# Kernel optimization log

Measured on AMD Instinct MI355X. Metric: run time of the kernel, lower is better.

Reference implementation:

```python
import jax, jax.numpy as jnp
import numpy as np

B, D, C = 8192, 2048, 1000
NUM_IDS = 256
MSEL_W, ORTH_W, CONS_W = 0.5, 0.1, 0.1


def setup_inputs() -> dict:
    key = jax.random.key(0)
    ks = jax.random.split(key, 7)
    return {
        "feat_shared": jax.random.normal(ks[0], (B, D), dtype=jnp.float32),
        "dee1": jax.random.normal(ks[1], (B, D), dtype=jnp.float32),
        "dee2": jax.random.normal(ks[2], (B, D), dtype=jnp.float32),
        "dee3": jax.random.normal(ks[3], (B, D), dtype=jnp.float32),
        "logits": jax.random.normal(ks[4], (B, C), dtype=jnp.float32),
        "labels": jax.random.randint(ks[5], (B,), 0, NUM_IDS, dtype=jnp.int32),
        "modal_ids": jax.random.randint(ks[6], (B,), 0, 2, dtype=jnp.int32),
    }


def _l2norm(x):
    return x / jnp.sqrt(jnp.sum(x * x, axis=1, keepdims=True)).clip(1e-12)


def _msel(features, labels, modal_ids):
    f = _l2norm(features)
    m_rgb = (modal_ids == 0).astype(f.dtype)  # [B]
    m_sar = (modal_ids == 1).astype(f.dtype)
    # per-label per-modal sums and counts via segment_sum (fixed NUM_IDS segments)
    sum_rgb = jax.ops.segment_sum(f * m_rgb[:, None], labels, num_segments=NUM_IDS)  # [L,D]
    sum_sar = jax.ops.segment_sum(f * m_sar[:, None], labels, num_segments=NUM_IDS)
    n_rgb = jax.ops.segment_sum(m_rgb, labels, num_segments=NUM_IDS)  # [L]
    n_sar = jax.ops.segment_sum(m_sar, labels, num_segments=NUM_IDS)
    c_rgb = sum_rgb / jnp.maximum(n_rgb, 1.0)[:, None]
    c_sar = sum_sar / jnp.maximum(n_sar, 1.0)[:, None]
    dist_cross = 1.0 - jnp.sum(c_rgb * c_sar, axis=1)
    # mean of Gram(f_rgb, f_rgb) == center_rgb . center_rgb (includes diagonal), same math
    dist_intra = 1.0 - jnp.sum(c_rgb * c_rgb, axis=1)
    valid = (n_rgb >= 2.0) & (n_sar >= 1.0)
    per_label = jnp.where(valid, (dist_cross - dist_intra) ** 2, 0.0)
    count = jnp.sum(valid.astype(f.dtype))
    return jnp.where(count > 0, jnp.sum(per_label) / jnp.maximum(count, 1.0), 0.0)


def _orth(f1, f2, f3):
    n1, n2, n3 = _l2norm(f1), _l2norm(f2), _l2norm(f3)
    s12 = jnp.mean(jnp.abs(jnp.sum(n1 * n2, axis=1)))
    s13 = jnp.mean(jnp.abs(jnp.sum(n1 * n3, axis=1)))
    s23 = jnp.mean(jnp.abs(jnp.sum(n2 * n3, axis=1)))
    return s12 + s13 + s23


def _consistency(logits, modal_ids):
    probs = jax.nn.softmax(logits, axis=1)  # [B,C]
    m_rgb = (modal_ids == 0).astype(probs.dtype)
    m_sar = (modal_ids == 1).astype(probs.dtype)
    n_rgb = jnp.sum(m_rgb)
    n_sar = jnp.sum(m_sar)
    p_rgb = jnp.sum(probs * m_rgb[:, None], axis=0) / jnp.maximum(n_rgb, 1.0)
    p_sar = jnp.sum(probs * m_sar[:, None], axis=0) / jnp.maximum(n_sar, 1.0)
    lr, ls = jnp.log(p_rgb), jnp.log(p_sar)
    # F.kl_div(log p, q, 'sum') = sum q*(log q - log p)
    kl = 0.5 * (jnp.sum(p_sar * (ls - lr)) + jnp.sum(p_rgb * (lr - ls)))
    return jnp.where((n_rgb > 0) & (n_sar > 0), kl, 0.0)


def reference(feat_shared, dee1, dee2, dee3, logits, labels, modal_ids):
    loss = MSEL_W * _msel(feat_shared, labels, modal_ids)
    loss = loss + ORTH_W * _orth(dee1, dee2, dee3)
    loss = loss + CONS_W * _consistency(logits, modal_ids)
    return loss
```

## Files before the change

kernel.cpp:

```cpp
#include <hip/hip_runtime.h>
#include <math.h>

#define B_   8192
#define D_   2048
#define C_   1000
#define L_   256
#define BIN_CAP 64

#define BIN_BLK  32
#define ORTH_BLK 512
#define NORM_BLK 128
#define CONS_BLK 128
#define GRID_ (BIN_BLK + ORTH_BLK + NORM_BLK + CONS_BLK)
#define ORTH_WAVES (ORTH_BLK * 4)

typedef unsigned short bf16raw;

__device__ __forceinline__ float bflo(unsigned int u) { return __uint_as_float(u << 16); }
__device__ __forceinline__ float bfhi(unsigned int u) { return __uint_as_float(u & 0xffff0000u); }

__device__ __forceinline__ bf16raw f2b(float f) {
  unsigned int x = __float_as_uint(f);
  unsigned int r = (x + 0x7fffu + ((x >> 16) & 1u)) >> 16;
  return (bf16raw)r;
}

__device__ __forceinline__ void dec8(uint4 u, float* x) {
  x[0] = bflo(u.x); x[1] = bfhi(u.x);
  x[2] = bflo(u.y); x[3] = bfhi(u.y);
  x[4] = bflo(u.z); x[5] = bfhi(u.z);
  x[6] = bflo(u.w); x[7] = bfhi(u.w);
}

__device__ __forceinline__ float waveSum(float v) {
#pragma unroll
  for (int off = 32; off > 0; off >>= 1) v += __shfl_xor(v, off, 64);
  return v;
}

__device__ __forceinline__ float blockSum(float v, float* lds4) {
  v = waveSum(v);
  const int wave = threadIdx.x >> 6;
  if ((threadIdx.x & 63) == 0) lds4[wave] = v;
  __syncthreads();
  v = lds4[0] + lds4[1] + lds4[2] + lds4[3];
  __syncthreads();
  return v;
}

__device__ __forceinline__ int detect_isb(const unsigned int* feat_words, float* lds4) {
  const unsigned int w = feat_words[threadIdx.x];
  const float a = fabsf(bflo(w));
  float hit = (a > 1e-3f && a < 10.f) ? 1.f : 0.f;
  hit = blockSum(hit, lds4);
  return hit > 128.f ? 1 : 0;
}

__global__ __launch_bounds__(256) void init_kernel(int* counts, float* accs,
                                                   float* p_final) {
  const int t = blockIdx.x * 256 + threadIdx.x;
  if (t < 2 * L_) counts[t] = 0;
  if (t < 16) accs[t] = 0.f;
  if (t < 2 * C_) p_final[t] = 0.f;
}

__device__ __forceinline__ void ldrow3(const bf16raw* pa, const bf16raw* pb,
                                       const bf16raw* pc, size_t base, int lane,
                                       uint4 (&A)[4], uint4 (&Bv)[4], uint4 (&Cv)[4]) {
  const uint4* qa = (const uint4*)(pa + base);
  const uint4* qb = (const uint4*)(pb + base);
  const uint4* qc = (const uint4*)(pc + base);
#pragma unroll
  for (int j = 0; j < 4; ++j) A[j] = qa[j * 64 + lane];
#pragma unroll
  for (int j = 0; j < 4; ++j) Bv[j] = qb[j * 64 + lane];
#pragma unroll
  for (int j = 0; j < 4; ++j) Cv[j] = qc[j * 64 + lane];
}

__device__ __forceinline__ void orth_rowacc(const uint4 (&A)[4], const uint4 (&Bv)[4],
                                            const uint4 (&Cv)[4], float (&v)[6]) {
#pragma unroll
  for (int j = 0; j < 4; ++j) {
    float a[8], b[8], c[8];
    dec8(A[j], a); dec8(Bv[j], b); dec8(Cv[j], c);
#pragma unroll
    for (int k = 0; k < 8; ++k) {
      v[0] += a[k] * a[k]; v[1] += b[k] * b[k]; v[2] += c[k] * c[k];
      v[3] += a[k] * b[k]; v[4] += a[k] * c[k]; v[5] += b[k] * c[k];
    }
  }
}

__device__ __forceinline__ float ssq4(const uint4 (&X)[4]) {
  float ss = 0.f;
#pragma unroll
  for (int j = 0; j < 4; ++j) {
    float x[8]; dec8(X[j], x);
#pragma unroll
    for (int k = 0; k < 8; ++k) ss += x[k] * x[k];
  }
  return ss;
}

__device__ __forceinline__ void loadlogits_f32(const void* logits, int r, int lane,
                                               float (&x)[16]) {
#pragma unroll
  for (int kk = 0; kk < 4; ++kk) {
    const int idx = lane + (kk << 6);
    if (idx < (C_ / 4)) {
      const float4 w = ((const float4*)((const float*)logits + (size_t)r * C_))[idx];
      x[4 * kk + 0] = w.x; x[4 * kk + 1] = w.y;
      x[4 * kk + 2] = w.z; x[4 * kk + 3] = w.w;
    } else {
      x[4 * kk + 0] = -INFINITY; x[4 * kk + 1] = -INFINITY;
      x[4 * kk + 2] = -INFINITY; x[4 * kk + 3] = -INFINITY;
    }
  }
}

__device__ __forceinline__ void softmax_acc(float (&x)[16], int m, float (&accA)[16],
                                            float (&accB)[16]) {
  float mx = -INFINITY;
#pragma unroll
  for (int k = 0; k < 16; ++k) mx = fmaxf(mx, x[k]);
#pragma unroll
  for (int off = 32; off > 0; off >>= 1) mx = fmaxf(mx, __shfl_xor(mx, off, 64));
  float s = 0.f;
#pragma unroll
  for (int k = 0; k < 16; ++k) { x[k] = expf(x[k] - mx); s += x[k]; }
#pragma unroll
  for (int off = 32; off > 0; off >>= 1) s += __shfl_xor(s, off, 64);
  const float inv = 1.f / s;
  if (m == 0) {
#pragma unroll
    for (int k = 0; k < 16; ++k) accA[k] += x[k] * inv;
  } else {
#pragma unroll
    for (int k = 0; k < 16; ++k) accB[k] += x[k] * inv;
  }
}

__global__ __launch_bounds__(256) void fused_main_kernel(
    const void* feat, const void* f1, const void* f2, const void* f3,
    const void* logits, const int* labels, const int* modal,
    int* counts, int* rowlist, float* orth_part, float* norms, float* p_final) {
  __shared__ float wacc[4][2][1024];
  __shared__ float lds4[4];
  const int t = threadIdx.x;
  const int wave = t >> 6, lane = t & 63;
  const int isb = detect_isb((const unsigned int*)feat, lds4);
  const int bx = blockIdx.x;

  if (bx < BIN_BLK) {
    const int r = bx * 256 + t;
    const int m = modal[r] ? 1 : 0;
    int lb = labels[r]; lb = lb < 0 ? 0 : (lb >= L_ ? L_ - 1 : lb);
    const int key = m * L_ + lb;
    const int idx = atomicAdd(&counts[key], 1);
    if (idx < BIN_CAP) rowlist[key * BIN_CAP + idx] = r;
  } else if (bx < BIN_BLK + ORTH_BLK) {
    const int gw = (bx - BIN_BLK) * 4 + wave;
    float s12 = 0.f, s13 = 0.f, s23 = 0.f;
    if (isb) {
      const bf16raw* pa = (const bf16raw*)f1;
      const bf16raw* pb = (const bf16raw*)f2;
      const bf16raw* pc = (const bf16raw*)f3;
      for (int r = 0; r < 4; ++r) {
        const size_t base = ((size_t)gw * 4 + r) * D_;
        uint4 A[4], Bv[4], Cv[4];
        ldrow3(pa, pb, pc, base, lane, A, Bv, Cv);
        float v[6] = {0.f, 0.f, 0.f, 0.f, 0.f, 0.f};
        orth_rowacc(A, Bv, Cv, v);
#pragma unroll
        for (int off = 32; off > 0; off >>= 1) {
#pragma unroll
          for (int j = 0; j < 6; ++j) v[j] += __shfl_xor(v[j], off, 64);
        }
        const float q1 = fmaxf(sqrtf(v[0]), 1e-12f);
        const float q2 = fmaxf(sqrtf(v[1]), 1e-12f);
        const float q3 = fmaxf(sqrtf(v[2]), 1e-12f);
        s12 += fabsf(v[3]) / (q1 * q2);
        s13 += fabsf(v[4]) / (q1 * q3);
        s23 += fabsf(v[5]) / (q2 * q3);
      }
    } else {
      for (int r = 0; r < 4; ++r) {
        const size_t base = ((size_t)gw * 4 + r) * D_;
        const float4* qa = (const float4*)((const float*)f1 + base);
        const float4* qb = (const float4*)((const float*)f2 + base);
        const float4* qc = (const float4*)((const float*)f3 + base);
        float v[6] = {0.f, 0.f, 0.f, 0.f, 0.f, 0.f};
#pragma unroll
        for (int h = 0; h < 8; ++h) {
          const float4 a4 = qa[h * 64 + lane];
          const float4 b4 = qb[h * 64 + lane];
          const float4 c4 = qc[h * 64 + lane];
          const float a[4] = {a4.x, a4.y, a4.z, a4.w};
          const float b[4] = {b4.x, b4.y, b4.z, b4.w};
          const float c[4] = {c4.x, c4.y, c4.z, c4.w};
#pragma unroll
          for (int k = 0; k < 4; ++k) {
            v[0] += a[k] * a[k]; v[1] += b[k] * b[k]; v[2] += c[k] * c[k];
            v[3] += a[k] * b[k]; v[4] += a[k] * c[k]; v[5] += b[k] * c[k];
          }
        }
#pragma unroll
        for (int off = 32; off > 0; off >>= 1) {
#pragma unroll
          for (int j = 0; j < 6; ++j) v[j] += __shfl_xor(v[j], off, 64);
        }
        const float q1 = fmaxf(sqrtf(v[0]), 1e-12f);
        const float q2 = fmaxf(sqrtf(v[1]), 1e-12f);
        const float q3 = fmaxf(sqrtf(v[2]), 1e-12f);
        s12 += fabsf(v[3]) / (q1 * q2);
        s13 += fabsf(v[4]) / (q1 * q3);
        s23 += fabsf(v[5]) / (q2 * q3);
      }
    }
    if (lane == 0) {
      orth_part[gw] = s12;
      orth_part[ORTH_WAVES + gw] = s13;
      orth_part[2 * ORTH_WAVES + gw] = s23;
    }
  } else if (bx < BIN_BLK + ORTH_BLK + NORM_BLK) {
    const int gw = (bx - BIN_BLK - ORTH_BLK) * 4 + wave;
    const size_t base0 = (size_t)gw * (16 * D_);
    if (isb) {
      const bf16raw* pf = (const bf16raw*)feat;
      for (int r = 0; r < 16; ++r) {
        const uint4* q = (const uint4*)(pf + base0 + (size_t)r * D_);
        uint4 X[4];
#pragma unroll
        for (int j = 0; j < 4; ++j) X[j] = q[j * 64 + lane];
        float ss = ssq4(X);
        ss = waveSum(ss);
        if (lane == 0) norms[gw * 16 + r] = 1.f / fmaxf(sqrtf(ss), 1e-12f);
      }
    } else {
      for (int r = 0; r < 16; ++r) {
        const float4* q = (const float4*)((const float*)feat + base0 + (size_t)r * D_);
        float ss = 0.f;
#pragma unroll
        for (int j = 0; j < 8; ++j) {
          const float4 w = q[j * 64 + lane];
          ss += w.x * w.x + w.y * w.y + w.z * w.z + w.w * w.w;
        }
        ss = waveSum(ss);
        if (lane == 0) norms[gw * 16 + r] = 1.f / fmaxf(sqrtf(ss), 1e-12f);
      }
    }
  } else {
    const int cb = bx - BIN_BLK - ORTH_BLK - NORM_BLK;
    const int rbase = cb * 64 + wave * 16;
    float accA[16], accB[16];
#pragma unroll
    for (int k = 0; k < 16; ++k) { accA[k] = 0.f; accB[k] = 0.f; }
    if (isb) {
      const bf16raw* pl = (const bf16raw*)logits;
      uint4 W0a, W1a;
      uint4 W0b = make_uint4(0u, 0u, 0u, 0u), W1b = make_uint4(0u, 0u, 0u, 0u);
      int ma, mb = 0;
      {
        const uint4* q = (const uint4*)(pl + (size_t)rbase * C_);
        W0a = q[lane];
        W1a = (lane < 61) ? q[64 + lane] : make_uint4(0u, 0u, 0u, 0u);
        ma = modal[rbase];
      }
      for (int i = 0; i < 16; ++i) {
        if (i < 15) {
          const int rn = rbase + i + 1;
          const uint4* q = (const uint4*)(pl + (size_t)rn * C_);
          W0b = q[lane];
          W1b = (lane < 61) ? q[64 + lane] : make_uint4(0u, 0u, 0u, 0u);
          mb = modal[rn];
        }
        float x[16];
        dec8(W0a, x);
        if (lane < 61) {
          float xx[8]; dec8(W1a, xx);
#pragma unroll
          for (int k = 0; k < 8; ++k) x[8 + k] = xx[k];
        } else {
#pragma unroll
          for (int k = 0; k < 8; ++k) x[8 + k] = -INFINITY;
        }
        softmax_acc(x, ma, accA, accB);
        W0a = W0b; W1a = W1b; ma = mb;
      }
#pragma unroll
      for (int k = 0; k < 16; ++k) {
        const int c = (k < 8) ? (8 * lane + k) : (512 + 8 * lane + (k - 8));
        wacc[wave][0][c] = accA[k];
        wacc[wave][1][c] = accB[k];
      }
    } else {
      float xa[16], xb[16];
      int ma, mb = 0;
      loadlogits_f32(logits, rbase, lane, xa);
      ma = modal[rbase];
      for (int i = 0; i < 16; ++i) {
        if (i < 15) {
          loadlogits_f32(logits, rbase + i + 1, lane, xb);
          mb = modal[rbase + i + 1];
        }
        softmax_acc(xa, ma, accA, accB);
#pragma unroll
        for (int k = 0; k < 16; ++k) xa[k] = xb[k];
        ma = mb;
      }
#pragma unroll
      for (int k = 0; k < 16; ++k) {
        const int c = 4 * (lane + ((k >> 2) << 6)) + (k & 3);
        wacc[wave][0][c] = accA[k];
        wacc[wave][1][c] = accB[k];
      }
    }
    __syncthreads();
    for (int e = t; e < 2 * C_; e += 256) {
      const int m = (e < C_) ? 0 : 1;
      const int c = e - m * C_;
      atomicAdd(&p_final[e],
                wacc[0][m][c] + wacc[1][m][c] + wacc[2][m][c] + wacc[3][m][c]);
    }
  }
}

__global__ __launch_bounds__(256) void label_kernel(const void* feat, const int* counts,
                                                    const int* rowlist, const float* norms,
                                                    float* accs) {
  __shared__ float lds4[4];
  const int l = blockIdx.x;
  const int t = threadIdx.x;
  const int isb = detect_isb((const unsigned int*)feat, lds4);
  const int nr_true = counts[l];
  const int ns_true = counts[L_ + l];
  const int nr = nr_true < BIN_CAP ? nr_true : BIN_CAP;
  const int ns = ns_true < BIN_CAP ? ns_true : BIN_CAP;
  const int tot = nr + ns;
  float accR[8], accS[8];
#pragma unroll
  for (int j = 0; j < 8; ++j) { accR[j] = 0.f; accS[j] = 0.f; }

  if (tot > 0) {
    auto rowAt = [&](int i) -> int {
      const int key = (i < nr) ? l : (L_ + l);
      const int idx = (i < nr) ? i : (i - nr);
      return rowlist[key * BIN_CAP + idx];
    };
    if (isb) {
      const bf16raw* pf = (const bf16raw*)feat;
      const int r0 = rowAt(0);
      uint4 qa = ((const uint4*)(pf + (size_t)r0 * D_))[t];
      float na = norms[r0];
      uint4 qb = make_uint4(0u, 0u, 0u, 0u);
      float nb2 = 0.f;
      if (tot > 1) {
        const int r1 = rowAt(1);
        qb = ((const uint4*)(pf + (size_t)r1 * D_))[t];
        nb2 = norms[r1];
      }
      for (int i = 0; i < tot; i += 2) {
        uint4 qc = make_uint4(0u, 0u, 0u, 0u), qd = make_uint4(0u, 0u, 0u, 0u);
        float nc = 0.f, nd = 0.f;
        if (i + 2 < tot) {
          const int rc = rowAt(i + 2);
          qc = ((const uint4*)(pf + (size_t)rc * D_))[t];
          nc = norms[rc];
        }
        if (i + 3 < tot) {
          const int rd = rowAt(i + 3);
          qd = ((const uint4*)(pf + (size_t)rd * D_))[t];
          nd = norms[rd];
        }
        {
          float x[8]; dec8(qa, x);
          if (i < nr) {
#pragma unroll
            for (int j = 0; j < 8; ++j) accR[j] += x[j] * na;
          } else {
#pragma unroll
            for (int j = 0; j < 8; ++j) accS[j] += x[j] * na;
          }
        }
        if (i + 1 < tot) {
          float x[8]; dec8(qb, x);
          if (i + 1 < nr) {
#pragma unroll
            for (int j = 0; j < 8; ++j) accR[j] += x[j] * nb2;
          } else {
#pragma unroll
            for (int j = 0; j < 8; ++j) accS[j] += x[j] * nb2;
          }
        }
        qa = qc; qb = qd; na = nc; nb2 = nd;
      }
    } else {
      const float* pf = (const float*)feat;
      const int r0 = rowAt(0);
      float4 a0 = ((const float4*)(pf + (size_t)r0 * D_))[2 * t];
      float4 a1 = ((const float4*)(pf + (size_t)r0 * D_))[2 * t + 1];
      float na = norms[r0];
      float4 b0 = make_float4(0.f, 0.f, 0.f, 0.f), b1 = make_float4(0.f, 0.f, 0.f, 0.f);
      float nb2 = 0.f;
      if (tot > 1) {
        const int r1 = rowAt(1);
        b0 = ((const float4*)(pf + (size_t)r1 * D_))[2 * t];
        b1 = ((const float4*)(pf + (size_t)r1 * D_))[2 * t + 1];
        nb2 = norms[r1];
      }
      for (int i = 0; i < tot; i += 2) {
        float4 c0 = make_float4(0.f, 0.f, 0.f, 0.f), c1 = c0, d0 = c0, d1 = c0;
        float nc = 0.f, nd = 0.f;
        if (i + 2 < tot) {
          const int rc = rowAt(i + 2);
          c0 = ((const float4*)(pf + (size_t)rc * D_))[2 * t];
          c1 = ((const float4*)(pf + (size_t)rc * D_))[2 * t + 1];
          nc = norms[rc];
        }
        if (i + 3 < tot) {
          const int rd = rowAt(i + 3);
          d0 = ((const float4*)(pf + (size_t)rd * D_))[2 * t];
          d1 = ((const float4*)(pf + (size_t)rd * D_))[2 * t + 1];
          nd = norms[rd];
        }
        {
          const float x[8] = {a0.x, a0.y, a0.z, a0.w, a1.x, a1.y, a1.z, a1.w};
          if (i < nr) {
#pragma unroll
            for (int j = 0; j < 8; ++j) accR[j] += x[j] * na;
          } else {
#pragma unroll
            for (int j = 0; j < 8; ++j) accS[j] += x[j] * na;
          }
        }
        if (i + 1 < tot) {
          const float x[8] = {b0.x, b0.y, b0.z, b0.w, b1.x, b1.y, b1.z, b1.w};
          if (i + 1 < nr) {
#pragma unroll
            for (int j = 0; j < 8; ++j) accR[j] += x[j] * nb2;
          } else {
#pragma unroll
            for (int j = 0; j < 8; ++j) accS[j] += x[j] * nb2;
          }
        }
        a0 = c0; a1 = c1; b0 = d0; b1 = d1; na = nc; nb2 = nd;
      }
    }
  }
  float rr = 0.f, rs = 0.f;
#pragma unroll
  for (int j = 0; j < 8; ++j) { rr += accR[j] * accR[j]; rs += accR[j] * accS[j]; }
  rr = blockSum(rr, lds4);
  rs = blockSum(rs, lds4);
  if (t == 0 && nr_true >= 2 && ns_true >= 1) {
    const float fr = (float)nr_true, fs = (float)ns_true;
    const float diff = rr / (fr * fr) - rs / (fr * fs);
    atomicAdd(&accs[3], diff * diff);
    atomicAdd(&accs[4], 1.0f);
  }
}

__global__ __launch_bounds__(256) void InnovationLoss_88124138979690_kernel(
    const void* feat, const float* p_final, const int* counts, const float* accs,
    const float* orth_part, void* out) {
  __shared__ float lds4[4];
  const int t = threadIdx.x;
  const int isb = detect_isb((const unsigned int*)feat, lds4);
  const float nr = blockSum((float)counts[t], lds4);
  const float ns = blockSum((float)counts[L_ + t], lds4);
  const float fr = fmaxf(nr, 1.f), fs = fmaxf(ns, 1.f);
  float klp = 0.f;
  for (int c = t; c < C_; c += 256) {
    const float pr = p_final[c] / fr;
    const float ps = p_final[C_ + c] / fs;
    klp += (ps - pr) * (logf(ps) - logf(pr));
  }
  klp = blockSum(klp, lds4);
  float o0 = 0.f, o1 = 0.f, o2 = 0.f;
  for (int b = t; b < ORTH_WAVES; b += 256) {
    o0 += orth_part[b];
    o1 += orth_part[ORTH_WAVES + b];
    o2 += orth_part[2 * ORTH_WAVES + b];
  }
  o0 = blockSum(o0, lds4);
  o1 = blockSum(o1, lds4);
  o2 = blockSum(o2, lds4);
  if (t == 0) {
    const float kl = (nr > 0.f && ns > 0.f) ? 0.5f * klp : 0.f;
    const float msel_cnt = accs[4];
    const float msel = msel_cnt > 0.f ? accs[3] / fmaxf(msel_cnt, 1.f) : 0.f;
    const float orth = (o0 + o1 + o2) * (1.0f / (float)B_);
    const float res = 0.5f * msel + 0.1f * orth + 0.1f * kl;
    if (isb) ((bf16raw*)out)[0] = f2b(res);
    else     ((float*)out)[0]   = res;
  }
}

extern "C" __attribute__((visibility("default")))
void kernel_launch(void* const* d_in, const int* in_sizes, int n_in,
                   void* d_out, int out_size, void* d_ws, size_t ws_size,
                   hipStream_t stream) {
  const void* feat   = d_in[0];
  const void* dee1   = d_in[1];
  const void* dee2   = d_in[2];
  const void* dee3   = d_in[3];
  const void* logits = d_in[4];
  const int*  labels = (const int*)d_in[5];
  const int*  modal  = (const int*)d_in[6];

  char* ws = (char*)d_ws;
  int*   counts    = (int*)  (ws);
  float* accs      = (float*)(ws + 2048);
  float* p_final   = (float*)(ws + 2112);
  int*   rowlist   = (int*)  (ws + 10112);
  float* norms     = (float*)(ws + 141184);
  float* orth_part = (float*)(ws + 173952);

  init_kernel<<<8, 256, 0, stream>>>(counts, accs, p_final);
  fused_main_kernel<<<GRID_, 256, 0, stream>>>(feat, dee1, dee2, dee3, logits, labels,
                                               modal, counts, rowlist, orth_part, norms,
                                               p_final);
  label_kernel<<<L_, 256, 0, stream>>>(feat, counts, rowlist, norms, accs);
  InnovationLoss_88124138979690_kernel<<<1, 256, 0, stream>>>(feat, p_final, counts,
                                                              accs, orth_part, d_out);
}
```

Baseline: 306.8 us.

## Scatter normalized rows into per-label centers with atomics instead of label gather pass

During the row-norm pass, each normalized feature row is atomically added into a per-(modal,label) center buffer. A small reduce kernel then computes the center dot products, replacing the label kernel that re-reads binned feature rows. This removes the second read of feature data and the BIN_CAP limit, but adds 4M float atomics, a 4 MB zeroing pass, and a dependence on workspace size. It also changes the workspace offsets of norms and orth_part.

```diff
diff --git a/kernel.cpp b/kernel.cpp
--- a/kernel.cpp
+++ b/kernel.cpp
@@ -57,11 +57,15 @@
 }
 
 __global__ __launch_bounds__(256) void init_kernel(int* counts, float* accs,
-                                                   float* p_final) {
-  const int t = blockIdx.x * 256 + threadIdx.x;
-  if (t < 2 * L_) counts[t] = 0;
-  if (t < 16) accs[t] = 0.f;
-  if (t < 2 * C_) p_final[t] = 0.f;
+                                                   float* p_final, float* centers,
+                                                   int do_centers) {
+  const int gid = blockIdx.x * 256 + threadIdx.x;
+  if (gid < 2 * L_) counts[gid] = 0;
+  if (gid < 16) accs[gid] = 0.f;
+  if (gid < 2 * C_) p_final[gid] = 0.f;
+  if (do_centers) {
+    for (int i = gid; i < 2 * L_ * D_; i += 1024 * 256) centers[i] = 0.f;
+  }
 }
 
 __device__ __forceinline__ void ldrow3(const bf16raw* pa, const bf16raw* pb,
@@ -144,7 +148,8 @@
 __global__ __launch_bounds__(256) void fused_main_kernel(
     const void* feat, const void* f1, const void* f2, const void* f3,
     const void* logits, const int* labels, const int* modal,
-    int* counts, int* rowlist, float* orth_part, float* norms, float* p_final) {
+    int* counts, int* rowlist, float* orth_part, float* norms, float* p_final,
+    float* centers, int do_centers) {
   __shared__ float wacc[4][2][1024];
   __shared__ float lds4[4];
   const int t = threadIdx.x;
@@ -225,29 +230,59 @@
     }
   } else if (bx < BIN_BLK + ORTH_BLK + NORM_BLK) {
     const int gw = (bx - BIN_BLK - ORTH_BLK) * 4 + wave;
-    const size_t base0 = (size_t)gw * (16 * D_);
     if (isb) {
       const bf16raw* pf = (const bf16raw*)feat;
       for (int r = 0; r < 16; ++r) {
-        const uint4* q = (const uint4*)(pf + base0 + (size_t)r * D_);
+        const int row = gw * 16 + r;
+        const uint4* q = (const uint4*)(pf + (size_t)row * D_);
         uint4 X[4];
 #pragma unroll
         for (int j = 0; j < 4; ++j) X[j] = q[j * 64 + lane];
         float ss = ssq4(X);
         ss = waveSum(ss);
-        if (lane == 0) norms[gw * 16 + r] = 1.f / fmaxf(sqrtf(ss), 1e-12f);
+        const float invn = 1.f / fmaxf(sqrtf(ss), 1e-12f);
+        if (lane == 0) norms[row] = invn;
+        if (do_centers) {
+          int lb = labels[row]; lb = lb < 0 ? 0 : (lb >= L_ ? L_ - 1 : lb);
+          const int m = modal[row] ? 1 : 0;
+          float* cb = centers + (size_t)(m * L_ + lb) * D_;
+#pragma unroll
+          for (int j = 0; j < 4; ++j) {
+            float x[8]; dec8(X[j], x);
+            const int e0 = (j * 64 + lane) * 8;
+#pragma unroll
+            for (int k = 0; k < 8; ++k) atomicAdd(&cb[e0 + k], x[k] * invn);
+          }
+        }
       }
     } else {
+      const float* pf = (const float*)feat;
       for (int r = 0; r < 16; ++r) {
-        const float4* q = (const float4*)((const float*)feat + base0 + (size_t)r * D_);
+        const int row = gw * 16 + r;
+        const float4* q = (const float4*)(pf + (size_t)row * D_);
+        float4 W[8];
         float ss = 0.f;
 #pragma unroll
         for (int j = 0; j < 8; ++j) {
-          const float4 w = q[j * 64 + lane];
-          ss += w.x * w.x + w.y * w.y + w.z * w.z + w.w * w.w;
+          W[j] = q[j * 64 + lane];
+          ss += W[j].x * W[j].x + W[j].y * W[j].y + W[j].z * W[j].z + W[j].w * W[j].w;
         }
         ss = waveSum(ss);
-        if (lane == 0) norms[gw * 16 + r] = 1.f / fmaxf(sqrtf(ss), 1e-12f);
+        const float invn = 1.f / fmaxf(sqrtf(ss), 1e-12f);
+        if (lane == 0) norms[row] = invn;
+        if (do_centers) {
+          int lb = labels[row]; lb = lb < 0 ? 0 : (lb >= L_ ? L_ - 1 : lb);
+          const int m = modal[row] ? 1 : 0;
+          float* cb = centers + (size_t)(m * L_ + lb) * D_;
+#pragma unroll
+          for (int j = 0; j < 8; ++j) {
+            const int e0 = (j * 64 + lane) * 4;
+            atomicAdd(&cb[e0 + 0], W[j].x * invn);
+            atomicAdd(&cb[e0 + 1], W[j].y * invn);
+            atomicAdd(&cb[e0 + 2], W[j].z * invn);
+            atomicAdd(&cb[e0 + 3], W[j].w * invn);
+          }
+        }
       }
     }
   } else {
@@ -322,6 +357,32 @@
       const int c = e - m * C_;
       atomicAdd(&p_final[e],
                 wacc[0][m][c] + wacc[1][m][c] + wacc[2][m][c] + wacc[3][m][c]);
+    }
+  }
+}
+
+__global__ __launch_bounds__(256) void reduce_kernel(const float* centers,
+                                                     const int* counts, float* accs) {
+  __shared__ float lds4[4];
+  const int l = blockIdx.x;
+  const int t = threadIdx.x;
+  const float* cr = centers + (size_t)l * D_;
+  const float* cs = centers + (size_t)(L_ + l) * D_;
+  float rr = 0.f, rs = 0.f;
+  for (int d = t; d < D_; d += 256) {
+    const float a = cr[d], b = cs[d];
+    rr += a * a;
+    rs += a * b;
+  }
+  rr = blockSum(rr, lds4);
+  rs = blockSum(rs, lds4);
+  if (t == 0) {
+    const int nr = counts[l], ns = counts[L_ + l];
+    if (nr >= 2 && ns >= 1) {
+      const float fr = (float)nr, fs = (float)ns;
+      const float diff = rr / (fr * fr) - rs / (fr * fs);
+      atomicAdd(&accs[3], diff * diff);
+      atomicAdd(&accs[4], 1.0f);
     }
   }
 }
@@ -514,14 +575,22 @@
   float* accs      = (float*)(ws + 2048);
   float* p_final   = (float*)(ws + 2112);
   int*   rowlist   = (int*)  (ws + 10112);
-  float* norms     = (float*)(ws + 141184);
-  float* orth_part = (float*)(ws + 173952);
-
-  init_kernel<<<8, 256, 0, stream>>>(counts, accs, p_final);
+  float* orth_part = (float*)(ws + 141184);
+  float* norms     = (float*)(ws + 165760);
+  float* centers   = (float*)(ws + 198656);
+  const int use_scatter = (ws_size >= (size_t)198656 + 2 * L_ * D_ * sizeof(float)) ? 1 : 0;
+  float* centers_arg = use_scatter ? centers : (float*)(ws + 2048);
+
+  init_kernel<<<use_scatter ? 1024 : 8, 256, 0, stream>>>(counts, accs, p_final,
+                                                          centers_arg, use_scatter);
   fused_main_kernel<<<GRID_, 256, 0, stream>>>(feat, dee1, dee2, dee3, logits, labels,
                                                modal, counts, rowlist, orth_part, norms,
-                                               p_final);
-  label_kernel<<<L_, 256, 0, stream>>>(feat, counts, rowlist, norms, accs);
+                                               p_final, centers_arg, use_scatter);
+  if (use_scatter) {
+    reduce_kernel<<<L_, 256, 0, stream>>>(centers, counts, accs);
+  } else {
+    label_kernel<<<L_, 256, 0, stream>>>(feat, counts, rowlist, norms, accs);
+  }
   InnovationLoss_88124138979690_kernel<<<1, 256, 0, stream>>>(feat, p_final, counts,
                                                               accs, orth_part, d_out);
 }
```

Measured after the change: 475.9 us. 1.55x slower.

## Rebalance fused kernel block split with grid-stride rows and staged row lists

Applied to the files above, without the earlier changes.

Changes the per-role block counts of the fused main kernel (more orthogonality, norm and consistency blocks) and converts each role to grid-stride row loops instead of fixed contiguous chunks. Orthogonality partial sums are now reduced per block in shared memory, so there are fewer partials for the final kernel to sum. The per-label centroid kernel now stages row indices and inverse norms in shared memory once, rather than recomputing the list lookup and reading norms from global memory inside the loop. Grid-stride loops leave some waves with uneven row counts, and the extra block-level sync adds a small overhead.

```diff
diff --git a/kernel.cpp b/kernel.cpp
--- a/kernel.cpp
+++ b/kernel.cpp
@@ -8,11 +8,13 @@
 #define BIN_CAP 64
 
 #define BIN_BLK  32
-#define ORTH_BLK 512
-#define NORM_BLK 128
-#define CONS_BLK 128
+#define ORTH_BLK 640
+#define NORM_BLK 192
+#define CONS_BLK 160
 #define GRID_ (BIN_BLK + ORTH_BLK + NORM_BLK + CONS_BLK)
-#define ORTH_WAVES (ORTH_BLK * 4)
+#define ORTH_W (ORTH_BLK * 4)
+#define NORM_W (NORM_BLK * 4)
+#define CONS_W (CONS_BLK * 4)
 
 typedef unsigned short bf16raw;
 
@@ -147,6 +149,7 @@
     int* counts, int* rowlist, float* orth_part, float* norms, float* p_final) {
   __shared__ float wacc[4][2][1024];
   __shared__ float lds4[4];
+  __shared__ float osum[4][3];
   const int t = threadIdx.x;
   const int wave = t >> 6, lane = t & 63;
   const int isb = detect_isb((const unsigned int*)feat, lds4);
@@ -160,14 +163,15 @@
     const int idx = atomicAdd(&counts[key], 1);
     if (idx < BIN_CAP) rowlist[key * BIN_CAP + idx] = r;
   } else if (bx < BIN_BLK + ORTH_BLK) {
-    const int gw = (bx - BIN_BLK) * 4 + wave;
+    const int ob = bx - BIN_BLK;
+    const int gw = ob * 4 + wave;
     float s12 = 0.f, s13 = 0.f, s23 = 0.f;
     if (isb) {
       const bf16raw* pa = (const bf16raw*)f1;
       const bf16raw* pb = (const bf16raw*)f2;
       const bf16raw* pc = (const bf16raw*)f3;
-      for (int r = 0; r < 4; ++r) {
-        const size_t base = ((size_t)gw * 4 + r) * D_;
+      for (int row = gw; row < B_; row += ORTH_W) {
+        const size_t base = (size_t)row * D_;
         uint4 A[4], Bv[4], Cv[4];
         ldrow3(pa, pb, pc, base, lane, A, Bv, Cv);
         float v[6] = {0.f, 0.f, 0.f, 0.f, 0.f, 0.f};
@@ -185,8 +189,8 @@
         s23 += fabsf(v[5]) / (q2 * q3);
       }
     } else {
-      for (int r = 0; r < 4; ++r) {
-        const size_t base = ((size_t)gw * 4 + r) * D_;
+      for (int row = gw; row < B_; row += ORTH_W) {
+        const size_t base = (size_t)row * D_;
         const float4* qa = (const float4*)((const float*)f1 + base);
         const float4* qb = (const float4*)((const float*)f2 + base);
         const float4* qc = (const float4*)((const float*)f3 + base);
@@ -218,28 +222,28 @@
         s23 += fabsf(v[5]) / (q2 * q3);
       }
     }
-    if (lane == 0) {
-      orth_part[gw] = s12;
-      orth_part[ORTH_WAVES + gw] = s13;
-      orth_part[2 * ORTH_WAVES + gw] = s23;
+    if (lane == 0) { osum[wave][0] = s12; osum[wave][1] = s13; osum[wave][2] = s23; }
+    __syncthreads();
+    if (t < 3) {
+      orth_part[t * ORTH_BLK + ob] = osum[0][t] + osum[1][t] + osum[2][t] + osum[3][t];
     }
   } else if (bx < BIN_BLK + ORTH_BLK + NORM_BLK) {
     const int gw = (bx - BIN_BLK - ORTH_BLK) * 4 + wave;
-    const size_t base0 = (size_t)gw * (16 * D_);
     if (isb) {
       const bf16raw* pf = (const bf16raw*)feat;
-      for (int r = 0; r < 16; ++r) {
-        const uint4* q = (const uint4*)(pf + base0 + (size_t)r * D_);
+      for (int row = gw; row < B_; row += NORM_W) {
+        const uint4* q = (const uint4*)(pf + (size_t)row * D_);
         uint4 X[4];
 #pragma unroll
         for (int j = 0; j < 4; ++j) X[j] = q[j * 64 + lane];
         float ss = ssq4(X);
         ss = waveSum(ss);
-        if (lane == 0) norms[gw * 16 + r] = 1.f / fmaxf(sqrtf(ss), 1e-12f);
+        if (lane == 0) norms[row] = 1.f / fmaxf(sqrtf(ss), 1e-12f);
       }
     } else {
-      for (int r = 0; r < 16; ++r) {
-        const float4* q = (const float4*)((const float*)feat + base0 + (size_t)r * D_);
+      const float* pf = (const float*)feat;
+      for (int row = gw; row < B_; row += NORM_W) {
+        const float4* q = (const float4*)(pf + (size_t)row * D_);
         float ss = 0.f;
 #pragma unroll
         for (int j = 0; j < 8; ++j) {
@@ -247,12 +251,12 @@
           ss += w.x * w.x + w.y * w.y + w.z * w.z + w.w * w.w;
         }
         ss = waveSum(ss);
-        if (lane == 0) norms[gw * 16 + r] = 1.f / fmaxf(sqrtf(ss), 1e-12f);
+        if (lane == 0) norms[row] = 1.f / fmaxf(sqrtf(ss), 1e-12f);
       }
     }
   } else {
     const int cb = bx - BIN_BLK - ORTH_BLK - NORM_BLK;
-    const int rbase = cb * 64 + wave * 16;
+    const int gw = cb * 4 + wave;
     float accA[16], accB[16];
 #pragma unroll
     for (int k = 0; k < 16; ++k) { accA[k] = 0.f; accB[k] = 0.f; }
@@ -262,14 +266,14 @@
       uint4 W0b = make_uint4(0u, 0u, 0u, 0u), W1b = make_uint4(0u, 0u, 0u, 0u);
       int ma, mb = 0;
       {
-        const uint4* q = (const uint4*)(pl + (size_t)rbase * C_);
+        const uint4* q = (const uint4*)(pl + (size_t)gw * C_);
         W0a = q[lane];
         W1a = (lane < 61) ? q[64 + lane] : make_uint4(0u, 0u, 0u, 0u);
-        ma = modal[rbase];
-      }
-      for (int i = 0; i < 16; ++i) {
-        if (i < 15) {
-          const int rn = rbase + i + 1;
+        ma = modal[gw];
+      }
+      for (int r = gw; r < B_; r += CONS_W) {
+        const int rn = r + CONS_W;
+        if (rn < B_) {
           const uint4* q = (const uint4*)(pl + (size_t)rn * C_);
           W0b = q[lane];
           W1b = (lane < 61) ? q[64 + lane] : make_uint4(0u, 0u, 0u, 0u);
@@ -297,12 +301,13 @@
     } else {
       float xa[16], xb[16];
       int ma, mb = 0;
-      loadlogits_f32(logits, rbase, lane, xa);
-      ma = modal[rbase];
-      for (int i = 0; i < 16; ++i) {
-        if (i < 15) {
-          loadlogits_f32(logits, rbase + i + 1, lane, xb);
-          mb = modal[rbase + i + 1];
+      loadlogits_f32(logits, gw, lane, xa);
+      ma = modal[gw];
+      for (int r = gw; r < B_; r += CONS_W) {
+        const int rn = r + CONS_W;
+        if (rn < B_) {
+          loadlogits_f32(logits, rn, lane, xb);
+          mb = modal[rn];
         }
         softmax_acc(xa, ma, accA, accB);
 #pragma unroll
@@ -330,6 +335,8 @@
                                                     const int* rowlist, const float* norms,
                                                     float* accs) {
   __shared__ float lds4[4];
+  __shared__ int   slist[2 * BIN_CAP];
+  __shared__ float snorm[2 * BIN_CAP];
   const int l = blockIdx.x;
   const int t = threadIdx.x;
   const int isb = detect_isb((const unsigned int*)feat, lds4);
@@ -338,40 +345,39 @@
   const int nr = nr_true < BIN_CAP ? nr_true : BIN_CAP;
   const int ns = ns_true < BIN_CAP ? ns_true : BIN_CAP;
   const int tot = nr + ns;
+  if (t < tot) {
+    const int key = (t < nr) ? l : (L_ + l);
+    const int idx = (t < nr) ? t : (t - nr);
+    const int r = rowlist[key * BIN_CAP + idx];
+    slist[t] = r;
+    snorm[t] = norms[r];
+  }
+  __syncthreads();
   float accR[8], accS[8];
 #pragma unroll
   for (int j = 0; j < 8; ++j) { accR[j] = 0.f; accS[j] = 0.f; }
 
   if (tot > 0) {
-    auto rowAt = [&](int i) -> int {
-      const int key = (i < nr) ? l : (L_ + l);
-      const int idx = (i < nr) ? i : (i - nr);
-      return rowlist[key * BIN_CAP + idx];
-    };
     if (isb) {
       const bf16raw* pf = (const bf16raw*)feat;
-      const int r0 = rowAt(0);
-      uint4 qa = ((const uint4*)(pf + (size_t)r0 * D_))[t];
-      float na = norms[r0];
+      uint4 qa = ((const uint4*)(pf + (size_t)slist[0] * D_))[t];
+      float na = snorm[0];
       uint4 qb = make_uint4(0u, 0u, 0u, 0u);
       float nb2 = 0.f;
       if (tot > 1) {
-        const int r1 = rowAt(1);
-        qb = ((const uint4*)(pf + (size_t)r1 * D_))[t];
-        nb2 = norms[r1];
+        qb = ((const uint4*)(pf + (size_t)slist[1] * D_))[t];
+        nb2 = snorm[1];
       }
       for (int i = 0; i < tot; i += 2) {
         uint4 qc = make_uint4(0u, 0u, 0u, 0u), qd = make_uint4(0u, 0u, 0u, 0u);
         float nc = 0.f, nd = 0.f;
         if (i + 2 < tot) {
-          const int rc = rowAt(i + 2);
-          qc = ((const uint4*)(pf + (size_t)rc * D_))[t];
-          nc = norms[rc];
+          qc = ((const uint4*)(pf + (size_t)slist[i + 2] * D_))[t];
+          nc = snorm[i + 2];
         }
         if (i + 3 < tot) {
-          const int rd = rowAt(i + 3);
-          qd = ((const uint4*)(pf + (size_t)rd * D_))[t];
-          nd = norms[rd];
+          qd = ((const uint4*)(pf + (size_t)slist[i + 3] * D_))[t];
+          nd = snorm[i + 3];
         }
         {
           float x[8]; dec8(qa, x);
@@ -397,32 +403,28 @@
       }
     } else {
       const float* pf = (const float*)feat;
-      const int r0 = rowAt(0);
-      float4 a0 = ((const float4*)(pf + (size_t)r0 * D_))[2 * t];
-      float4 a1 = ((const float4*)(pf + (size_t)r0 * D_))[2 * t + 1];
-      float na = norms[r0];
+      float4 a0 = ((const float4*)(pf + (size_t)slist[0] * D_))[2 * t];
+      float4 a1 = ((const float4*)(pf + (size_t)slist[0] * D_))[2 * t + 1];
+      float na = snorm[0];
       float4 b0 = make_float4(0.f, 0.f, 0.f, 0.f), b1 = make_float4(0.f, 0.f, 0.f, 0.f);
       float nb2 = 0.f;
       if (tot > 1) {
-        const int r1 = rowAt(1);
-        b0 = ((const float4*)(pf + (size_t)r1 * D_))[2 * t];
-        b1 = ((const float4*)(pf + (size_t)r1 * D_))[2 * t + 1];
-        nb2 = norms[r1];
+        b0 = ((const float4*)(pf + (size_t)slist[1] * D_))[2 * t];
+        b1 = ((const float4*)(pf + (size_t)slist[1] * D_))[2 * t + 1];
+        nb2 = snorm[1];
       }
       for (int i = 0; i < tot; i += 2) {
         float4 c0 = make_float4(0.f, 0.f, 0.f, 0.f), c1 = c0, d0 = c0, d1 = c0;
         float nc = 0.f, nd = 0.f;
         if (i + 2 < tot) {
-          const int rc = rowAt(i + 2);
-          c0 = ((const float4*)(pf + (size_t)rc * D_))[2 * t];
-          c1 = ((const float4*)(pf + (size_t)rc * D_))[2 * t + 1];
-          nc = norms[rc];
+          c0 = ((const float4*)(pf + (size_t)slist[i + 2] * D_))[2 * t];
+          c1 = ((const float4*)(pf + (size_t)slist[i + 2] * D_))[2 * t + 1];
+          nc = snorm[i + 2];
         }
         if (i + 3 < tot) {
-          const int rd = rowAt(i + 3);
-          d0 = ((const float4*)(pf + (size_t)rd * D_))[2 * t];
-          d1 = ((const float4*)(pf + (size_t)rd * D_))[2 * t + 1];
-          nd = norms[rd];
+          d0 = ((const float4*)(pf + (size_t)slist[i + 3] * D_))[2 * t];
+          d1 = ((const float4*)(pf + (size_t)slist[i + 3] * D_))[2 * t + 1];
+          nd = snorm[i + 3];
         }
         {
           const float x[8] = {a0.x, a0.y, a0.z, a0.w, a1.x, a1.y, a1.z, a1.w};
@@ -478,10 +480,10 @@
   }
   klp = blockSum(klp, lds4);
   float o0 = 0.f, o1 = 0.f, o2 = 0.f;
-  for (int b = t; b < ORTH_WAVES; b += 256) {
+  for (int b = t; b < ORTH_BLK; b += 256) {
     o0 += orth_part[b];
-    o1 += orth_part[ORTH_WAVES + b];
-    o2 += orth_part[2 * ORTH_WAVES + b];
+    o1 += orth_part[ORTH_BLK + b];
+    o2 += orth_part[2 * ORTH_BLK + b];
   }
   o0 = blockSum(o0, lds4);
   o1 = blockSum(o1, lds4);
```

Result: no change. 312.7 us (+1.9%).
